# Kernel optimization log

Measured on AMD Instinct MI355X. Metric: run time of the kernel, lower is better.

The kernel has to match this reference:

```python
import jax, jax.numpy as jnp
import numpy as np

EPS = 1e-5
B, N, NPOINT, K = 16, 4096, 1024, 32
IN_CH, OUT_CH = 64, 64


def index_points(points, idx):
    # points: [B, N, C], idx: [B, ...] -> [B, ..., C]
    b = points.shape[0]
    flat = idx.reshape(b, -1)
    out = jnp.take_along_axis(points, flat[:, :, None], axis=1)
    return out.reshape(idx.shape + (points.shape[-1],))


def bn2d(x, gamma, beta):
    # x: [B, C, H, W], batch-stat BN (training mode), biased variance
    m = x.mean(axis=(0, 2, 3), keepdims=True)
    v = x.var(axis=(0, 2, 3), keepdims=True)
    return gamma[None, :, None, None] * (x - m) / jnp.sqrt(v + EPS) + beta[None, :, None, None]


def bn1d(x, gamma, beta):
    # x: [B, C, L]
    m = x.mean(axis=(0, 2), keepdims=True)
    v = x.var(axis=(0, 2), keepdims=True)
    return gamma[None, :, None] * (x - m) / jnp.sqrt(v + EPS) + beta[None, :, None]


def conv1x1(x, w, b):
    # x: [B, C, H, W], w: [O, C], b: [O]
    return jnp.einsum('bchw,oc->bohw', x, w) + b[None, :, None, None]


def setup_inputs() -> dict:
    key = jax.random.key(0)
    ks = jax.random.split(key, 16)
    inp = {
        'xyz': jax.random.normal(ks[0], (B, N, 3), jnp.float32),
        'points': jax.random.normal(ks[1], (B, N, 61), jnp.float32),
        'local_coordinates': jax.random.normal(ks[2], (B, NPOINT * K, 3), jnp.float32),
        'neighbor_lists': jax.random.randint(ks[3], (B, NPOINT, K), 0, N),
        'data_idx': jax.random.randint(ks[4], (B, NPOINT), 0, N),
        # WeightNet: 3 -> 16 -> 16 -> OUT_CH, each conv1x1 + BN2d + relu
        'w0': jax.random.normal(ks[5], (16, 3), jnp.float32) * 0.1,
        'b0': jnp.zeros((16,), jnp.float32),
        'g0': jnp.ones((16,), jnp.float32),
        'be0': jnp.zeros((16,), jnp.float32),
        'w1': jax.random.normal(ks[6], (16, 16), jnp.float32) * 0.1,
        'b1': jnp.zeros((16,), jnp.float32),
        'g1': jnp.ones((16,), jnp.float32),
        'be1': jnp.zeros((16,), jnp.float32),
        'w2': jax.random.normal(ks[7], (OUT_CH, 16), jnp.float32) * 0.1,
        'b2': jnp.zeros((OUT_CH,), jnp.float32),
        'g2': jnp.ones((OUT_CH,), jnp.float32),
        'be2': jnp.zeros((OUT_CH,), jnp.float32),
        # bn_conv over IN_CH*OUT_CH channels
        'gc': jnp.ones((IN_CH * OUT_CH,), jnp.float32),
        'bc': jnp.zeros((IN_CH * OUT_CH,), jnp.float32),
        # linear IN_CH*OUT_CH -> OUT_CH
        'lw': jax.random.normal(ks[8], (IN_CH * OUT_CH, OUT_CH), jnp.float32) * 0.01,
        'lb': jnp.zeros((OUT_CH,), jnp.float32),
        # bn_linear
        'gl': jnp.ones((OUT_CH,), jnp.float32),
        'bl': jnp.zeros((OUT_CH,), jnp.float32),
    }
    return inp


def reference(xyz, points, local_coordinates, neighbor_lists, data_idx,
              w0, b0, g0, be0, w1, b1, g1, be1, w2, b2, g2, be2,
              gc, bc, lw, lb, gl, bl):
    new_xyz = index_points(xyz, data_idx)                       # [B, NPOINT, 3]
    pts = jnp.concatenate([points, xyz], axis=2)                # [B, N, IN_CH]
    grouped = index_points(pts, neighbor_lists)                 # [B, NPOINT, K, IN_CH]
    grouped = grouped.transpose(0, 1, 3, 2)                     # [B, NPOINT, IN_CH, K]

    # WeightNet on local coordinates
    lc = local_coordinates.reshape(B, NPOINT, K, 3).transpose(0, 3, 2, 1)  # [B, 3, K, NPOINT]
    h = jax.nn.relu(bn2d(conv1x1(lc, w0, b0), g0, be0))
    h = jax.nn.relu(bn2d(conv1x1(h, w1, b1), g1, be1))
    h = jax.nn.relu(bn2d(conv1x1(h, w2, b2), g2, be2))          # [B, OUT_CH, K, NPOINT]
    weights = h.transpose(0, 3, 2, 1)                            # [B, NPOINT, K, OUT_CH]

    # aggregate over neighbors: [B, NPOINT, IN_CH, OUT_CH]
    new_points = jnp.einsum('bnik,bnko->bnio', grouped, weights)
    new_points = new_points.reshape(B, NPOINT, IN_CH * OUT_CH)

    new_points = jax.nn.relu(
        bn1d(new_points.transpose(0, 2, 1), gc, bc).transpose(0, 2, 1))
    new_points = new_points @ lw + lb                            # [B, NPOINT, OUT_CH]
    new_points = bn1d(new_points.transpose(0, 2, 1), gl, bl).transpose(0, 2, 1)
    new_points = jax.nn.relu(new_points)
    return (new_xyz, new_points)
```

## Files before the change

### kernel.cpp

```cpp
#include <hip/hip_runtime.h>
#include <hip/hip_bf16.h>

#define BB 16
#define NN 4096
#define NPOINTS 1024
#define KK 32
#define NPTS (BB*NPOINTS)
#define NWN  (BB*NPOINTS*KK)
#define EPSF 1e-5f
#define SGBLK 512
#define SGIT  4

typedef unsigned short u16;
typedef u16  u16x8 __attribute__((ext_vector_type(8)));
typedef short s16x8 __attribute__((ext_vector_type(8)));
typedef float f32x4 __attribute__((ext_vector_type(4)));
typedef float f32x4u __attribute__((ext_vector_type(4), aligned(4)));

__device__ __forceinline__ float bf(u16 u){
  union { unsigned int i; float f; } v; v.i = ((unsigned int)u) << 16; return v.f;
}
__device__ __forceinline__ u16 f2b(float f){
  __hip_bfloat16 h = __float2bfloat16(f);
  union { __hip_bfloat16 hh; u16 u; } v; v.hh = h; return v.u;
}


__global__ __launch_bounds__(256) void k_init(const float* xyz, const int* didx, float* out,
                                              const float* lw, u16* lwbt){
  int t = threadIdx.x;
  if (blockIdx.x < 64){
    int p = blockIdx.x * 256 + t;
    int b = p >> 10;
    int idx = didx[p];
    const float* src = xyz + ((size_t)(b * NN + idx)) * 3;
    float* dst = out + (size_t)p * 3;
    dst[0] = src[0]; dst[1] = src[1]; dst[2] = src[2];
  } else {
    __shared__ float T[64][65];
    int kb = (blockIdx.x - 64) * 64;
    {
      int k = t >> 2, c4 = t & 3;
      #pragma unroll
      for (int j = 0; j < 4; ++j)
        *(f32x4*)&T[k][c4*16 + j*4] = *(const f32x4*)(lw + (size_t)(kb + k)*64 + c4*16 + j*4);
    }
    __syncthreads();
    {
      int n = t >> 2, k4 = t & 3;
      u16x8 o0, o1;
      #pragma unroll
      for (int j = 0; j < 8; ++j) o0[j] = f2b(T[k4*16 + j][n]);
      #pragma unroll
      for (int j = 0; j < 8; ++j) o1[j] = f2b(T[k4*16 + 8 + j][n]);
      *(u16x8*)(lwbt + (size_t)n*4096 + kb + k4*16)     = o0;
      *(u16x8*)(lwbt + (size_t)n*4096 + kb + k4*16 + 8) = o1;
    }
  }
}

__global__ __launch_bounds__(256) void k_stat0(const float* lc, float* PA){
  int t = threadIdx.x;
  float a[9];
  #pragma unroll
  for (int r = 0; r < 9; ++r) a[r] = 0.f;
  size_t base = (size_t)blockIdx.x * 1024 + t;
  for (int ip = 0; ip < 4; ++ip){
    size_t p = base + (size_t)ip * 256;
    float x0 = lc[p*3], x1 = lc[p*3+1], x2 = lc[p*3+2];
    a[0]+=x0; a[1]+=x1; a[2]+=x2;
    a[3]+=x0*x0; a[4]+=x0*x1; a[5]+=x0*x2;
    a[6]+=x1*x1; a[7]+=x1*x2; a[8]+=x2*x2;
  }
  #pragma unroll
  for (int m = 1; m < 64; m <<= 1){
    #pragma unroll
    for (int r = 0; r < 9; ++r) a[r] += __shfl_xor(a[r], m);
  }
  if ((t & 63) == 0){
    float* dst = PA + (size_t)(blockIdx.x*4 + (t>>6)) * 16;
    f32x4 v0 = {a[0],a[1],a[2],a[3]}, v1 = {a[4],a[5],a[6],a[7]}, v2 = {a[8],0.f,0.f,0.f};
    *(f32x4*)dst = v0; *(f32x4*)(dst+4) = v1; *(f32x4*)(dst+8) = v2;
  }
}

__global__ __launch_bounds__(256) void k_red0(const float* PA, const float* w0, const float* b0,
                                              const float* g0, const float* be0, float* F){
  __shared__ float ms[12];
  __shared__ float a0sh[16];
  int t = threadIdx.x;
  if (t < 12){
    float s0=0,s1=0,s2=0,s3=0;
    const float* p = PA + t;
    for (int r = 0; r < 2048; r += 4){
      s0 += p[(size_t)(r+0)*16]; s1 += p[(size_t)(r+1)*16];
      s2 += p[(size_t)(r+2)*16]; s3 += p[(size_t)(r+3)*16];
    }
    ms[t] = (s0+s1)+(s2+s3);
  }
  __syncthreads();
  if (t < 16){
    float wx = w0[t*3], wy = w0[t*3+1], wz = w0[t*3+2], bb = b0[t];
    float lin = wx*ms[0] + wy*ms[1] + wz*ms[2];
    float quad = wx*wx*ms[3] + wy*wy*ms[6] + wz*wz*ms[8]
               + 2.f*(wx*wy*ms[4] + wx*wz*ms[5] + wy*wz*ms[7]);
    float S = lin + (float)NWN * bb;
    float Q = quad + 2.f*bb*lin + (float)NWN*bb*bb;
    float m = S * (1.f/NWN);
    float v = Q * (1.f/NWN) - m*m;
    float a = g0[t] * rsqrtf(v + EPSF);
    float d = be0[t] - m*a;
    a0sh[t] = a;
    F[48+t] = a*bb + d;
  }
  __syncthreads();
  if (t < 48) F[t] = a0sh[t/3] * w0[t];
}

template<bool L2>
__global__ __launch_bounds__(256) void k_statG(const float* lc, const float* F, float* PB){
  __shared__ f32x4 w0p[16];
  __shared__ float w1s[256], b1fs[16];
  __shared__ __align__(16) u16 Ht[4][16*72];
  __shared__ float GS[4][16][17];
  __shared__ float SHs[4][16];
  int t = threadIdx.x;
  int w = t >> 6, l = t & 63;
  if (t < 16){
    f32x4 wv = {F[t*3], F[t*3+1], F[t*3+2], F[48+t]};
    w0p[t] = wv;
    if (L2) b1fs[t] = F[320+t];
  }
  if (L2) w1s[t] = F[64+t];
  __syncthreads();
  f32x4 acc = {0.f,0.f,0.f,0.f};
  float sh[16];
  #pragma unroll
  for (int r = 0; r < 16; ++r) sh[r] = 0.f;
  u16* Hw = &Ht[w][0];
  for (int it = 0; it < SGIT; ++it){
    size_t p = (size_t)blockIdx.x * (SGIT*256) + (size_t)it*256 + w*64 + l;
    float x0 = lc[p*3], x1 = lc[p*3+1], x2 = lc[p*3+2];
    float h[16];
    #pragma unroll
    for (int oc = 0; oc < 16; ++oc){
      f32x4 wv = w0p[oc];
      h[oc] = fmaxf(0.f, wv.x*x0 + wv.y*x1 + wv.z*x2 + wv.w);
    }
    if (L2){
      float h1[16];
      #pragma unroll
      for (int oc = 0; oc < 16; ++oc){
        const f32x4* wr = (const f32x4*)&w1s[oc*16];
        f32x4 wa = wr[0], wb = wr[1], wc = wr[2], wd = wr[3];
        float y = b1fs[oc];
        y += wa.x*h[0]  + wa.y*h[1]  + wa.z*h[2]  + wa.w*h[3];
        y += wb.x*h[4]  + wb.y*h[5]  + wb.z*h[6]  + wb.w*h[7];
        y += wc.x*h[8]  + wc.y*h[9]  + wc.z*h[10] + wc.w*h[11];
        y += wd.x*h[12] + wd.y*h[13] + wd.z*h[14] + wd.w*h[15];
        h1[oc] = fmaxf(0.f, y);
      }
      #pragma unroll
      for (int oc = 0; oc < 16; ++oc) h[oc] = h1[oc];
    }
    #pragma unroll
    for (int oc = 0; oc < 16; ++oc) sh[oc] += h[oc];
    #pragma unroll
    for (int c = 0; c < 16; ++c) Hw[c*72 + l] = f2b(h[c]);
    __syncthreads();
    #pragma unroll
    for (int tt = 0; tt < 2; ++tt){
      s16x8 af = *(const s16x8*)&Hw[(l & 15)*72 + tt*32 + (l >> 4)*8];
      acc = __builtin_amdgcn_mfma_f32_16x16x32_bf16(af, af, acc, 0, 0, 0);
    }
    __syncthreads();
  }
  #pragma unroll
  for (int r = 0; r < 4; ++r)
    GS[w][(l>>4)*4 + r][l & 15] = acc[r];
  #pragma unroll
  for (int m = 1; m < 64; m <<= 1){
    #pragma unroll
    for (int r = 0; r < 16; ++r) sh[r] += __shfl_xor(sh[r], m);
  }
  if (l == 0){
    #pragma unroll
    for (int r = 0; r < 16; ++r) SHs[w][r] = sh[r];
  }
  __syncthreads();
  {
    int i = t >> 4, j = t & 15;
    float g = GS[0][i][j] + GS[1][i][j] + GS[2][i][j] + GS[3][i][j];
    PB[(size_t)blockIdx.x*272 + t] = g;
    if (t < 16)
      PB[(size_t)blockIdx.x*272 + 256 + t] = SHs[0][t]+SHs[1][t]+SHs[2][t]+SHs[3][t];
  }
}

__global__ __launch_bounds__(256) void k_red1(const float* PB, const float* w1, const float* b1,
                                              const float* g1, const float* be1, float* F){
  __shared__ float red[272];
  __shared__ float a1sh[16];
  int t = threadIdx.x;
  for (int e = t; e < 272; e += 256){
    float s = 0.f;
    for (int r = 0; r < SGBLK; ++r) s += PB[(size_t)r*272 + e];
    red[e] = s;
  }
  __syncthreads();
  if (t < 16){
    float wv[16];
    #pragma unroll
    for (int ic = 0; ic < 16; ++ic) wv[ic] = w1[t*16+ic];
    float lin = 0.f;
    #pragma unroll
    for (int ic = 0; ic < 16; ++ic) lin += wv[ic]*red[256+ic];
    float quad = 0.f;
    for (int i = 0; i < 16; ++i){
      float ri = 0.f;
      #pragma unroll
      for (int j = 0; j < 16; ++j) ri += wv[j]*red[i*16+j];
      quad += wv[i]*ri;
    }
    float bb = b1[t];
    float S = lin + (float)NWN * bb;
    float Q = quad + 2.f*bb*lin + (float)NWN*bb*bb;
    float m = S * (1.f/NWN);
    float v = Q * (1.f/NWN) - m*m;
    float a = g1[t] * rsqrtf(v + EPSF);
    float d = be1[t] - m*a;
    a1sh[t] = a;
    F[320+t] = a*bb + d;
  }
  __syncthreads();
  F[64 + t] = a1sh[t >> 4] * w1[t];
}

__global__ __launch_bounds__(256) void k_red2(const float* PB, const float* w2, const float* b2,
                                              const float* g2, const float* be2, float* F){
  __shared__ float red[272];
  __shared__ float a2sh[64];
  int t = threadIdx.x;
  for (int e = t; e < 272; e += 256){
    float s = 0.f;
    for (int r = 0; r < SGBLK; ++r) s += PB[(size_t)r*272 + e];
    red[e] = s;
  }
  __syncthreads();
  if (t < 64){
    float wv[16];
    #pragma unroll
    for (int ic = 0; ic < 16; ++ic) wv[ic] = w2[t*16+ic];
    float lin = 0.f;
    #pragma unroll
    for (int ic = 0; ic < 16; ++ic) lin += wv[ic]*red[256+ic];
    float quad = 0.f;
    for (int i = 0; i < 16; ++i){
      float ri = 0.f;
      #pragma unroll
      for (int j = 0; j < 16; ++j) ri += wv[j]*red[i*16+j];
      quad += wv[i]*ri;
    }
    float bb = b2[t];
    float S = lin + (float)NWN * bb;
    float Q = quad + 2.f*bb*lin + (float)NWN*bb*bb;
    float m = S * (1.f/NWN);
    float v = Q * (1.f/NWN) - m*m;
    float a = g2[t] * rsqrtf(v + EPSF);
    float d = be2[t] - m*a;
    a2sh[t] = a;
    F[1360+t] = a*bb + d;
  }
  __syncthreads();
  for (int i = t; i < 1024; i += 256) F[336+i] = a2sh[i >> 4] * w2[i];
}

__global__ __launch_bounds__(256) void k_main(const float* lcg, const int* nbrg,
    const float* points, const float* xyz, const float* F,
    u16* npw){
  __shared__ u16   Gr[32*72];
  __shared__ u16   Wr[32*72];
  __shared__ float H0s[32][17];
  __shared__ float H1s[32][20];
  __shared__ float lcs[32][4];
  __shared__ int   nbr[32];
  __shared__ float w0c[48], b0c[16];
  __shared__ float w1c[16][17], b1c[16];
  __shared__ float w2c[64][17], b2c[64];
  int t = threadIdx.x;
  int point = blockIdx.x;
  int bb = point >> 10;
  if (t < 48) w0c[t] = F[t];
  if (t < 16){ b0c[t] = F[48+t]; b1c[t] = F[320+t]; }
  w1c[t>>4][t&15] = F[64+t];
  for (int i = t; i < 1024; i += 256) w2c[i>>4][i&15] = F[336+i];
  if (t < 64) b2c[t] = F[1360+t];
  if (t < 32) nbr[t] = nbrg[(size_t)point * 32 + t];
  if (t < 96){ int k = t / 3, c = t % 3; lcs[k][c] = lcg[(size_t)point * 96 + t]; }
  __syncthreads();

  {
    int k = t >> 3, c8 = t & 7;
    int n = nbr[k];
    const float* prow = points + (size_t)(bb * NN + n) * 61;
    u16x8 g;
    if (c8 < 7){
      f32x4 lo = *(const f32x4u*)(prow + c8*8);
      f32x4 hi = *(const f32x4u*)(prow + c8*8 + 4);
      g[0]=f2b(lo.x); g[1]=f2b(lo.y); g[2]=f2b(lo.z); g[3]=f2b(lo.w);
      g[4]=f2b(hi.x); g[5]=f2b(hi.y); g[6]=f2b(hi.z); g[7]=f2b(hi.w);
    } else {
      const float* xr = xyz + (size_t)(bb * NN + n) * 3;
      f32x4 lo = *(const f32x4u*)(prow + 56);
      g[0]=f2b(lo.x); g[1]=f2b(lo.y); g[2]=f2b(lo.z); g[3]=f2b(lo.w);
      g[4]=f2b(prow[60]);
      g[5]=f2b(xr[0]); g[6]=f2b(xr[1]); g[7]=f2b(xr[2]);
    }
    *(u16x8*)&Gr[k*72 + c8*8] = g;
  }
  #pragma unroll
  for (int jj = 0; jj < 2; ++jj){
    int l2 = t + jj * 256; int k = l2 >> 4, oc = l2 & 15;
    float y = w0c[oc*3]*lcs[k][0] + w0c[oc*3+1]*lcs[k][1] + w0c[oc*3+2]*lcs[k][2] + b0c[oc];
    H0s[k][oc] = fmaxf(0.f, y);
  }
  __syncthreads();
  #pragma unroll
  for (int jj = 0; jj < 2; ++jj){
    int l2 = t + jj * 256; int k = l2 >> 4, oc = l2 & 15;
    float y = b1c[oc];
    #pragma unroll
    for (int ic = 0; ic < 16; ++ic) y += w1c[oc][ic] * H0s[k][ic];
    H1s[k][oc] = fmaxf(0.f, y);
  }
  __syncthreads();
  {
    int o = t & 63, kb = (t >> 6) * 8;
    float wrow[16];
    #pragma unroll
    for (int ic = 0; ic < 16; ++ic) wrow[ic] = w2c[o][ic];
    float bb2 = b2c[o];
    #pragma unroll
    for (int j = 0; j < 8; ++j){
      const f32x4* hr = (const f32x4*)&H1s[kb + j][0];
      f32x4 h0v = hr[0], h1v = hr[1], h2v = hr[2], h3v = hr[3];
      float y = bb2;
      y += wrow[0]*h0v.x + wrow[1]*h0v.y + wrow[2]*h0v.z + wrow[3]*h0v.w;
      y += wrow[4]*h1v.x + wrow[5]*h1v.y + wrow[6]*h1v.z + wrow[7]*h1v.w;
      y += wrow[8]*h2v.x + wrow[9]*h2v.y + wrow[10]*h2v.z + wrow[11]*h2v.w;
      y += wrow[12]*h3v.x + wrow[13]*h3v.y + wrow[14]*h3v.z + wrow[15]*h3v.w;
      Wr[(kb + j)*72 + o] = f2b(fmaxf(0.f, y));
    }
  }
  __syncthreads();
  {
    int w = t >> 6, l = t & 63;
    int li = l & 15, lk = (l >> 4) * 8, lr = (l >> 4) * 4;
    s16x8 bfrag;
    #pragma unroll
    for (int j = 0; j < 8; ++j) bfrag[j] = (short)Wr[(lk + j)*72 + w*16 + li];
    #pragma unroll
    for (int it = 0; it < 4; ++it){
      s16x8 afrag;
      #pragma unroll
      for (int j = 0; j < 8; ++j) afrag[j] = (short)Gr[(lk + j)*72 + it*16 + li];
      f32x4 z = {0.f, 0.f, 0.f, 0.f};
      f32x4 d = __builtin_amdgcn_mfma_f32_16x16x32_bf16(afrag, bfrag, z, 0, 0, 0);
      #pragma unroll
      for (int r = 0; r < 4; ++r)
        npw[(size_t)point*4096 + (size_t)(it*16 + lr + r)*64 + w*16 + li] = f2b(d[r]);
    }
  }
}

__global__ __launch_bounds__(256) void k_statC(const u16* npw, float* PC){
  int t = threadIdx.x;
  float s[16], q[16];
  #pragma unroll
  for (int j = 0; j < 16; ++j){ s[j] = 0.f; q[j] = 0.f; }
  size_t rowbase = (size_t)blockIdx.x * 64;
  for (int p = 0; p < 64; ++p){
    const u16* row = npw + (rowbase + p) * 4096 + t * 16;
    u16x8 a = *(const u16x8*)row;
    u16x8 b = *(const u16x8*)(row + 8);
    #pragma unroll
    for (int j = 0; j < 8; ++j){ float v = bf(a[j]); s[j]   += v; q[j]   += v*v; }
    #pragma unroll
    for (int j = 0; j < 8; ++j){ float v = bf(b[j]); s[8+j] += v; q[8+j] += v*v; }
  }
  float* dst = PC + (size_t)blockIdx.x * 8192 + t * 16;
  #pragma unroll
  for (int j = 0; j < 16; ++j){ dst[j] = s[j]; dst[4096 + j] = q[j]; }
}

__global__ __launch_bounds__(256) void k_finC(const float* PC, const float* gc, const float* bc,
                                              float* AC, float* DC){
  int ch = blockIdx.x * 256 + threadIdx.x;
  float s = 0.f, q = 0.f;
  for (int r = 0; r < 256; ++r){
    s += PC[(size_t)r * 8192 + ch];
    q += PC[(size_t)r * 8192 + 4096 + ch];
  }
  float m = s * (1.f/16384.f);
  float v = q * (1.f/16384.f) - m*m;
  float a = gc[ch] * rsqrtf(v + EPSF);
  AC[ch] = a; DC[ch] = bc[ch] - m*a;
}

__global__ __launch_bounds__(256) void k_linear(const u16* npw, const float* AC, const float* DC,
                                                const u16* lwbt, const float* lb, float* yw,
                                                float* PL){
  __shared__ u16 Al[32*72];
  __shared__ u16 Bl[64*72];
  __shared__ float cps[64], cpq[64];
  int t = threadIdx.x;
  int w = t >> 6, l = t & 63;
  int rowbase = blockIdx.x * 32;
  int mt = w & 1, np2 = w >> 1;
  f32x4 acc0 = {0.f,0.f,0.f,0.f}, acc1 = acc0;
  for (int kb = 0; kb < 4096; kb += 64){
    __syncthreads();
    {
      int r = t >> 3, c8 = t & 7;
      int kk = kb + c8*8;
      u16x8 u = *(const u16x8*)(npw + (size_t)(rowbase + r)*4096 + kk);
      f32x4 alo = *(const f32x4*)(AC + kk), ahi = *(const f32x4*)(AC + kk + 4);
      f32x4 dlo = *(const f32x4*)(DC + kk), dhi = *(const f32x4*)(DC + kk + 4);
      u16x8 o;
      o[0] = f2b(fmaxf(0.f, alo.x*bf(u[0]) + dlo.x));
      o[1] = f2b(fmaxf(0.f, alo.y*bf(u[1]) + dlo.y));
      o[2] = f2b(fmaxf(0.f, alo.z*bf(u[2]) + dlo.z));
      o[3] = f2b(fmaxf(0.f, alo.w*bf(u[3]) + dlo.w));
      o[4] = f2b(fmaxf(0.f, ahi.x*bf(u[4]) + dhi.x));
      o[5] = f2b(fmaxf(0.f, ahi.y*bf(u[5]) + dhi.y));
      o[6] = f2b(fmaxf(0.f, ahi.z*bf(u[6]) + dhi.z));
      o[7] = f2b(fmaxf(0.f, ahi.w*bf(u[7]) + dhi.w));
      *(u16x8*)&Al[r*72 + c8*8] = o;
    }
    #pragma unroll
    for (int jj = 0; jj < 2; ++jj){
      int n = (t >> 3) + jj*32, c8 = t & 7;
      u16x8 u = *(const u16x8*)(lwbt + (size_t)n*4096 + kb + c8*8);
      *(u16x8*)&Bl[n*72 + c8*8] = u;
    }
    __syncthreads();
    #pragma unroll
    for (int ks = 0; ks < 2; ++ks){
      s16x8 af  = *(const s16x8*)&Al[(mt*16 + (l & 15))*72 + ks*32 + (l >> 4)*8];
      s16x8 bf0 = *(const s16x8*)&Bl[((np2*2    )*16 + (l & 15))*72 + ks*32 + (l >> 4)*8];
      s16x8 bf1 = *(const s16x8*)&Bl[((np2*2 + 1)*16 + (l & 15))*72 + ks*32 + (l >> 4)*8];
      acc0 = __builtin_amdgcn_mfma_f32_16x16x32_bf16(af, bf0, acc0, 0, 0, 0);
      acc1 = __builtin_amdgcn_mfma_f32_16x16x32_bf16(af, bf1, acc1, 0, 0, 0);
    }
  }
  int col0 = np2*32 + (l & 15), col1 = col0 + 16;
  float lb0 = lb[col0], lb1 = lb[col1];
  float s0 = 0.f, q0 = 0.f, s1 = 0.f, q1 = 0.f;
  if (t < 64){ cps[t] = 0.f; cpq[t] = 0.f; }
  __syncthreads();
  #pragma unroll
  for (int r = 0; r < 4; ++r){
    int row = rowbase + mt*16 + (l >> 4)*4 + r;
    float y0 = acc0[r] + lb0;
    float y1 = acc1[r] + lb1;
    yw[(size_t)row*64 + col0] = y0;
    yw[(size_t)row*64 + col1] = y1;
    s0 += y0; q0 += y0*y0; s1 += y1; q1 += y1*y1;
  }
  atomicAdd(&cps[col0], s0); atomicAdd(&cpq[col0], q0);
  atomicAdd(&cps[col1], s1); atomicAdd(&cpq[col1], q1);
  __syncthreads();
  if (t < 64){
    PL[blockIdx.x*128 + t]      = cps[t];
    PL[blockIdx.x*128 + 64 + t] = cpq[t];
  }
}

__global__ __launch_bounds__(128) void k_redF(const float* PL, float* SL){
  int t = threadIdx.x;
  float s = 0.f;
  for (int b = 0; b < 512; ++b) s += PL[b*128 + t];
  SL[t] = s;
}

__global__ __launch_bounds__(256) void k_final(const float* yw, const float* SL,
                                               const float* gl, const float* bl, float* out){
  int e = (blockIdx.x * 256 + threadIdx.x) * 4;
  int o = e & 63;
  f32x4 y = *(const f32x4*)(yw + e);
  f32x4 r;
  #pragma unroll
  for (int j = 0; j < 4; ++j){
    float m = SL[o+j] * (1.f/16384.f);
    float v = SL[64+o+j] * (1.f/16384.f) - m*m;
    float a = gl[o+j] * rsqrtf(v + EPSF);
    float d = bl[o+j] - m*a;
    r[j] = fmaxf(0.f, a*y[j] + d);
  }
  *(f32x4*)(out + 49152 + e) = r;
}

extern "C" void kernel_launch(void* const* d_in, const int* in_sizes, int n_in,
                              void* d_out, int out_size, void* d_ws, size_t ws_size,
                              hipStream_t stream){
  (void)in_sizes; (void)n_in; (void)out_size; (void)ws_size;
  const float* xyz    = (const float*)d_in[0];
  const float* points = (const float*)d_in[1];
  const float* lc     = (const float*)d_in[2];
  const int*   nbrl   = (const int*)d_in[3];
  const int*   didx   = (const int*)d_in[4];
  const float* w0 = (const float*)d_in[5];
  const float* b0 = (const float*)d_in[6];
  const float* g0 = (const float*)d_in[7];
  const float* be0= (const float*)d_in[8];
  const float* w1 = (const float*)d_in[9];
  const float* b1 = (const float*)d_in[10];
  const float* g1 = (const float*)d_in[11];
  const float* be1= (const float*)d_in[12];
  const float* w2 = (const float*)d_in[13];
  const float* b2 = (const float*)d_in[14];
  const float* g2 = (const float*)d_in[15];
  const float* be2= (const float*)d_in[16];
  const float* gc = (const float*)d_in[17];
  const float* bc = (const float*)d_in[18];
  const float* lw = (const float*)d_in[19];
  const float* lb = (const float*)d_in[20];
  const float* gl = (const float*)d_in[21];
  const float* bl = (const float*)d_in[22];
  float* out = (float*)d_out;
  char* ws = (char*)d_ws;

  float* F   = (float*)ws;
  float* SL  = F + 1536;
  float* AC  = SL + 128;
  float* DC  = AC + 4096;
  float* PA  = DC + 4096;
  float* PB1 = PA + 32768;
  float* PB2 = PB1 + 139264;
  float* PL  = PB2 + 139264;
  float* PC  = (float*)(ws + 4194304);
  u16*  npw  = (u16*)(ws + 4194304 + 8388608);
  float* yw  = (float*)(ws + 4194304 + 8388608 + 134217728);
  u16*  lwbt = (u16*)(ws + 4194304 + 8388608 + 134217728 + 4194304);

  k_init  <<<128,   256, 0, stream>>>(xyz, didx, out, lw, lwbt);
  k_stat0 <<<512,   256, 0, stream>>>(lc, PA);
  k_red0  <<<1,     256, 0, stream>>>(PA, w0, b0, g0, be0, F);
  k_statG<false><<<SGBLK, 256, 0, stream>>>(lc, F, PB1);
  k_red1  <<<1,     256, 0, stream>>>(PB1, w1, b1, g1, be1, F);
  k_statG<true> <<<SGBLK, 256, 0, stream>>>(lc, F, PB2);
  k_red2  <<<1,     256, 0, stream>>>(PB2, w2, b2, g2, be2, F);
  k_main  <<<16384, 256, 0, stream>>>(lc, nbrl, points, xyz, F, npw);
  k_statC <<<256,   256, 0, stream>>>(npw, PC);
  k_finC  <<<16,    256, 0, stream>>>(PC, gc, bc, AC, DC);
  k_linear<<<512,   256, 0, stream>>>(npw, AC, DC, lwbt, lb, yw, PL);
  k_redF  <<<1,     128, 0, stream>>>(PL, SL);
  k_final <<<1024,  256, 0, stream>>>(yw, SL, gl, bl, out);
}
```

Baseline: 282.2 us.

## Transpose intermediate layout to o-major and make WeightNet per-wave sync-free

The aggregated intermediate is now stored with the output channel as the major index, so each lane writes four contiguous bf16 values per MFMA tile instead of four scattered scalars. The linear weight transpose and the BN channel mapping in the finalize kernel are permuted to match. The WeightNet MLP is restructured so each wave handles its own 8 neighbors, reading neighbor indices and coordinates directly from global memory, which removes two block-wide barriers. The added risk is that every consumer must agree on the permuted channel order; the weight transpose now also uses scattered scalar stores.

```diff
diff --git a/kernel.cpp b/kernel.cpp
--- a/kernel.cpp
+++ b/kernel.cpp
@@ -13,6 +13,7 @@
 
 typedef unsigned short u16;
 typedef u16  u16x8 __attribute__((ext_vector_type(8)));
+typedef u16  u16x4 __attribute__((ext_vector_type(4)));
 typedef short s16x8 __attribute__((ext_vector_type(8)));
 typedef float f32x4 __attribute__((ext_vector_type(4)));
 typedef float f32x4u __attribute__((ext_vector_type(4), aligned(4)));
@@ -38,7 +39,8 @@
     dst[0] = src[0]; dst[1] = src[1]; dst[2] = src[2];
   } else {
     __shared__ float T[64][65];
-    int kb = (blockIdx.x - 64) * 64;
+    int ib = blockIdx.x - 64;
+    int kb = ib * 64;
     {
       int k = t >> 2, c4 = t & 3;
       #pragma unroll
@@ -48,13 +50,11 @@
     __syncthreads();
     {
       int n = t >> 2, k4 = t & 3;
-      u16x8 o0, o1;
-      #pragma unroll
-      for (int j = 0; j < 8; ++j) o0[j] = f2b(T[k4*16 + j][n]);
-      #pragma unroll
-      for (int j = 0; j < 8; ++j) o1[j] = f2b(T[k4*16 + 8 + j][n]);
-      *(u16x8*)(lwbt + (size_t)n*4096 + kb + k4*16)     = o0;
-      *(u16x8*)(lwbt + (size_t)n*4096 + kb + k4*16 + 8) = o1;
+      #pragma unroll
+      for (int j = 0; j < 16; ++j){
+        int k = k4*16 + j;
+        lwbt[(size_t)n*4096 + k*64 + ib] = f2b(T[k][n]);
+      }
     }
   }
 }
@@ -280,14 +280,13 @@
     u16* npw){
   __shared__ u16   Gr[32*72];
   __shared__ u16   Wr[32*72];
-  __shared__ float H0s[32][17];
-  __shared__ float H1s[32][20];
-  __shared__ float lcs[32][4];
-  __shared__ int   nbr[32];
+  __shared__ float H0s[4][8][17];
+  __shared__ float H1s[4][8][20];
   __shared__ float w0c[48], b0c[16];
   __shared__ float w1c[16][17], b1c[16];
   __shared__ float w2c[64][17], b2c[64];
   int t = threadIdx.x;
+  int w = t >> 6, l = t & 63;
   int point = blockIdx.x;
   int bb = point >> 10;
   if (t < 48) w0c[t] = F[t];
@@ -295,13 +294,11 @@
   w1c[t>>4][t&15] = F[64+t];
   for (int i = t; i < 1024; i += 256) w2c[i>>4][i&15] = F[336+i];
   if (t < 64) b2c[t] = F[1360+t];
-  if (t < 32) nbr[t] = nbrg[(size_t)point * 32 + t];
-  if (t < 96){ int k = t / 3, c = t % 3; lcs[k][c] = lcg[(size_t)point * 96 + t]; }
   __syncthreads();
 
   {
-    int k = t >> 3, c8 = t & 7;
-    int n = nbr[k];
+    int kg = w*8 + (l >> 3), c8 = l & 7;
+    int n = nbrg[(size_t)point*32 + kg];
     const float* prow = points + (size_t)(bb * NN + n) * 61;
     u16x8 g;
     if (c8 < 7){
@@ -316,49 +313,54 @@
       g[4]=f2b(prow[60]);
       g[5]=f2b(xr[0]); g[6]=f2b(xr[1]); g[7]=f2b(xr[2]);
     }
-    *(u16x8*)&Gr[k*72 + c8*8] = g;
-  }
-  #pragma unroll
-  for (int jj = 0; jj < 2; ++jj){
-    int l2 = t + jj * 256; int k = l2 >> 4, oc = l2 & 15;
-    float y = w0c[oc*3]*lcs[k][0] + w0c[oc*3+1]*lcs[k][1] + w0c[oc*3+2]*lcs[k][2] + b0c[oc];
-    H0s[k][oc] = fmaxf(0.f, y);
-  }
-  __syncthreads();
-  #pragma unroll
-  for (int jj = 0; jj < 2; ++jj){
-    int l2 = t + jj * 256; int k = l2 >> 4, oc = l2 & 15;
-    float y = b1c[oc];
-    #pragma unroll
-    for (int ic = 0; ic < 16; ++ic) y += w1c[oc][ic] * H0s[k][ic];
-    H1s[k][oc] = fmaxf(0.f, y);
-  }
-  __syncthreads();
+    *(u16x8*)&Gr[kg*72 + c8*8] = g;
+  }
   {
-    int o = t & 63, kb = (t >> 6) * 8;
+    int oc = l & 15;
+    #pragma unroll
+    for (int ee = 0; ee < 2; ++ee){
+      int kloc = (l >> 4) + ee*4;
+      const float* xp = lcg + (size_t)point*96 + (w*8 + kloc)*3;
+      float y = w0c[oc*3]*xp[0] + w0c[oc*3+1]*xp[1] + w0c[oc*3+2]*xp[2] + b0c[oc];
+      H0s[w][kloc][oc] = fmaxf(0.f, y);
+    }
+  }
+  {
+    int oc = l & 15;
+    #pragma unroll
+    for (int ee = 0; ee < 2; ++ee){
+      int kloc = (l >> 4) + ee*4;
+      float y = b1c[oc];
+      #pragma unroll
+      for (int ic = 0; ic < 16; ++ic) y += w1c[oc][ic] * H0s[w][kloc][ic];
+      H1s[w][kloc][oc] = fmaxf(0.f, y);
+    }
+  }
+  {
+    int o = l;
     float wrow[16];
     #pragma unroll
     for (int ic = 0; ic < 16; ++ic) wrow[ic] = w2c[o][ic];
     float bb2 = b2c[o];
     #pragma unroll
     for (int j = 0; j < 8; ++j){
-      const f32x4* hr = (const f32x4*)&H1s[kb + j][0];
+      const f32x4* hr = (const f32x4*)&H1s[w][j][0];
       f32x4 h0v = hr[0], h1v = hr[1], h2v = hr[2], h3v = hr[3];
       float y = bb2;
       y += wrow[0]*h0v.x + wrow[1]*h0v.y + wrow[2]*h0v.z + wrow[3]*h0v.w;
       y += wrow[4]*h1v.x + wrow[5]*h1v.y + wrow[6]*h1v.z + wrow[7]*h1v.w;
       y += wrow[8]*h2v.x + wrow[9]*h2v.y + wrow[10]*h2v.z + wrow[11]*h2v.w;
       y += wrow[12]*h3v.x + wrow[13]*h3v.y + wrow[14]*h3v.z + wrow[15]*h3v.w;
-      Wr[(kb + j)*72 + o] = f2b(fmaxf(0.f, y));
+      Wr[(w*8 + j)*72 + o] = f2b(fmaxf(0.f, y));
     }
   }
   __syncthreads();
   {
-    int w = t >> 6, l = t & 63;
     int li = l & 15, lk = (l >> 4) * 8, lr = (l >> 4) * 4;
     s16x8 bfrag;
     #pragma unroll
     for (int j = 0; j < 8; ++j) bfrag[j] = (short)Wr[(lk + j)*72 + w*16 + li];
+    size_t obase = (size_t)point*4096 + (size_t)(w*16 + li)*64 + lr;
     #pragma unroll
     for (int it = 0; it < 4; ++it){
       s16x8 afrag;
@@ -366,9 +368,9 @@
       for (int j = 0; j < 8; ++j) afrag[j] = (short)Gr[(lk + j)*72 + it*16 + li];
       f32x4 z = {0.f, 0.f, 0.f, 0.f};
       f32x4 d = __builtin_amdgcn_mfma_f32_16x16x32_bf16(afrag, bfrag, z, 0, 0, 0);
-      #pragma unroll
-      for (int r = 0; r < 4; ++r)
-        npw[(size_t)point*4096 + (size_t)(it*16 + lr + r)*64 + w*16 + li] = f2b(d[r]);
+      u16x4 st;
+      st[0] = f2b(d[0]); st[1] = f2b(d[1]); st[2] = f2b(d[2]); st[3] = f2b(d[3]);
+      *(u16x4*)(npw + obase + it*16) = st;
     }
   }
 }
@@ -395,16 +397,17 @@
 
 __global__ __launch_bounds__(256) void k_finC(const float* PC, const float* gc, const float* bc,
                                               float* AC, float* DC){
-  int ch = blockIdx.x * 256 + threadIdx.x;
+  int qpos = blockIdx.x * 256 + threadIdx.x;
   float s = 0.f, q = 0.f;
   for (int r = 0; r < 256; ++r){
-    s += PC[(size_t)r * 8192 + ch];
-    q += PC[(size_t)r * 8192 + 4096 + ch];
-  }
+    s += PC[(size_t)r * 8192 + qpos];
+    q += PC[(size_t)r * 8192 + 4096 + qpos];
+  }
+  int ch = (qpos & 63)*64 + (qpos >> 6);
   float m = s * (1.f/16384.f);
   float v = q * (1.f/16384.f) - m*m;
   float a = gc[ch] * rsqrtf(v + EPSF);
-  AC[ch] = a; DC[ch] = bc[ch] - m*a;
+  AC[qpos] = a; DC[qpos] = bc[ch] - m*a;
 }
 
 __global__ __launch_bounds__(256) void k_linear(const u16* npw, const float* AC, const float* DC,
```

Measured after the change: 287.5 us. No clear change (+1.9%).
